# Optimization experiments

Measured on AMD Instinct MI355X. Metric: run time of the kernel, lower is better.

## Reference

```python
import jax, jax.numpy as jnp
import numpy as np

B, T, C = 2, 2048, 1024
N_HEAD, D_HEAD = 16, 64


def setup_inputs() -> dict:
    key = jax.random.key(0)
    k1, k2, k3 = jax.random.split(key, 3)
    scale_in = 1.0 / np.sqrt(C)
    return {
        "x": jax.random.normal(k1, (B, T, C), dtype=jnp.float32),
        "W_attn": jax.random.normal(k2, (C, 3 * C), dtype=jnp.float32) * scale_in,
        "b_attn": jnp.zeros((3 * C,), dtype=jnp.float32),
        "W_proj": jax.random.normal(k3, (C, C), dtype=jnp.float32) * scale_in,
        "b_proj": jnp.zeros((C,), dtype=jnp.float32),
    }


def reference(x, W_attn, b_attn, W_proj, b_proj):
    Bx, Tx, Cx = x.shape
    qkv = x @ W_attn + b_attn                       # [B,T,3C]
    q, k, v = jnp.split(qkv, 3, axis=-1)
    # [B,T,C] -> [B,H,T,Dh]
    q = q.reshape(Bx, Tx, N_HEAD, D_HEAD).transpose(0, 2, 1, 3)
    k = k.reshape(Bx, Tx, N_HEAD, D_HEAD).transpose(0, 2, 1, 3)
    v = v.reshape(Bx, Tx, N_HEAD, D_HEAD).transpose(0, 2, 1, 3)
    att = jnp.einsum("bhqd,bhkd->bhqk", q, k) * (1.0 / jnp.sqrt(D_HEAD))
    causal_mask = jnp.tril(jnp.ones((Tx, Tx), dtype=jnp.bool_))[None, None]
    att = jnp.where(causal_mask, att, -jnp.inf)
    att = jax.nn.softmax(att, axis=-1)
    y = jnp.einsum("bhqk,bhkd->bhqd", att, v)        # [B,H,T,Dh]
    y = y.transpose(0, 2, 1, 3).reshape(Bx, Tx, Cx)  # [B,T,C]
    return y @ W_proj + b_proj
```

## Files before the change

### kernel.cpp

```cpp
#include <hip/hip_runtime.h>

#define BB 2
#define TT 2048
#define CC 1024
#define NHEAD 16
#define DHEAD 64

typedef __attribute__((ext_vector_type(8))) short short8;
typedef __attribute__((ext_vector_type(8))) unsigned short ushort8;
typedef __attribute__((ext_vector_type(4))) float floatx4;
typedef __attribute__((ext_vector_type(2))) unsigned int uintx2;

__device__ inline unsigned short f32_to_bf16_rne(float f) {
  unsigned u = __builtin_bit_cast(unsigned, f);
  unsigned r = (u + 0x7FFFu + ((u >> 16) & 1u)) >> 16;
  return (unsigned short)r;
}
__device__ inline unsigned cvt_pk_bf16(float lo, float hi) {
  unsigned r;
  asm("v_cvt_pk_bf16_f32 %0, %1, %2" : "=v"(r) : "v"(lo), "v"(hi));
  return r;
}
__device__ inline void gload_lds16(const void* g, void* l) {
  __builtin_amdgcn_global_load_lds(
      (const __attribute__((address_space(1))) void*)g,
      (__attribute__((address_space(3))) void*)l, 16, 0, 0);
}

__device__ inline void transpose_tile(const float* __restrict__ W,
                                      unsigned short* __restrict__ Wt,
                                      int K, int N, int scale_cut, float scl,
                                      int bx, int by, float (*T)[33]) {
  const int tx = threadIdx.x & 31;
  const int ty = threadIdx.x >> 5;
  const int r0 = by * 32, c0 = bx * 32;
#pragma unroll
  for (int i = 0; i < 4; ++i)
    T[ty + i * 8][tx] = W[(size_t)(r0 + ty + i * 8) * N + c0 + tx];
  __syncthreads();
#pragma unroll
  for (int i = 0; i < 4; ++i) {
    const int nrow = c0 + ty + i * 8;
    const float s = (nrow < scale_cut) ? scl : 1.0f;
    Wt[(size_t)nrow * K + r0 + tx] = f32_to_bf16_rne(T[tx][ty + i * 8] * s);
  }
}

__global__ __launch_bounds__(256) void prep_kernel(
    const float* __restrict__ x, const float* __restrict__ W_attn,
    const float* __restrict__ b_attn, const float* __restrict__ W_proj,
    unsigned short* __restrict__ xb, unsigned short* __restrict__ Wat,
    unsigned short* __restrict__ Wpt, float* __restrict__ bscl, float scl) {
  __shared__ float T[32][33];
  const int id = blockIdx.x;
  if (id < 4096) {
    const int i = (id * 256 + threadIdx.x) * 4;
    float4 v = *(const float4*)(x + i);
    ushort4 o;
    o.x = f32_to_bf16_rne(v.x);
    o.y = f32_to_bf16_rne(v.y);
    o.z = f32_to_bf16_rne(v.z);
    o.w = f32_to_bf16_rne(v.w);
    *(ushort4*)(xb + i) = o;
  } else if (id < 4096 + 3072) {
    const int t = id - 4096;
    transpose_tile(W_attn, Wat, CC, 3 * CC, CC, scl, t % 96, t / 96, T);
  } else if (id < 4096 + 3072 + 1024) {
    const int t = id - (4096 + 3072);
    transpose_tile(W_proj, Wpt, CC, CC, 0, 1.0f, t % 32, t / 32, T);
  } else {
    const int i = (id - 8192) * 256 + threadIdx.x;
    if (i < 3 * CC) bscl[i] = b_attn[i] * (i < CC ? scl : 1.0f);
  }
}

__global__ __launch_bounds__(256) void transpose_v_kernel(
    const unsigned short* __restrict__ qkv, unsigned short* __restrict__ vT) {
  __shared__ unsigned short Ts[64][72];
  const int tt0 = blockIdx.x * 64;
  const int bh = blockIdx.y;
  const int h = bh & (NHEAD - 1);
  const int b = bh >> 4;
  const int tid = threadIdx.x;
  const unsigned short* src = qkv + (size_t)(b * TT) * (3 * CC) + 2 * CC + h * DHEAD;
#pragma unroll
  for (int it = 0; it < 2; ++it) {
    const int t = it * 32 + (tid >> 3);
    const int d8 = (tid & 7) * 8;
    ushort8 v = *(const ushort8*)(src + (size_t)(tt0 + t) * (3 * CC) + d8);
#pragma unroll
    for (int j = 0; j < 8; ++j) Ts[t][d8 + j] = v[j];
  }
  __syncthreads();
  unsigned short* dst = vT + ((size_t)((b * NHEAD + h) * DHEAD)) * TT;
#pragma unroll
  for (int it = 0; it < 2; ++it) {
    const int d = it * 32 + (tid >> 3);
    const int t8 = (tid & 7) * 8;
    ushort8 o;
#pragma unroll
    for (int j = 0; j < 8; ++j) o[j] = Ts[t8 + j][d];
    *(ushort8*)(dst + (size_t)d * TT + tt0 + t8) = o;
  }
}

__global__ __launch_bounds__(512, 2) void gemm256_kernel(
    const unsigned short* __restrict__ A,
    const unsigned short* __restrict__ Bt,
    const float* __restrict__ bias,
    unsigned short* __restrict__ C,
    int M, int N, int K) {
  __shared__ unsigned short SA[3][256 * 32];
  __shared__ unsigned short SB[3][256 * 32];

  const int id = blockIdx.x;
  const int xcd = id & 7;
  const int j = id >> 3;
  const int row0 = (xcd * 2 + (j >= 12 ? 1 : 0)) * 256;
  const int col0 = (j % 12) * 256;

  const int tid = threadIdx.x;
  const int w = tid >> 6;
  const int lane = tid & 63;
  const int l15 = lane & 15;
  const int l4 = lane >> 4;
  const int wr = (w >> 2) * 128;
  const int wc = (w & 3) * 64;
  const int sr = lane >> 2;
  const int sc = lane & 3;

  floatx4 acc[8][4];
#pragma unroll
  for (int m = 0; m < 8; ++m)
#pragma unroll
    for (int n = 0; n < 4; ++n) acc[m][n] = (floatx4){0.f, 0.f, 0.f, 0.f};

  auto stageA = [&](int t) {
    const int buf = t % 3;
    const int k0 = t * 32;
#pragma unroll
    for (int l = 0; l < 2; ++l) {
      const int r = w * 16 + sr + l * 128;
      gload_lds16(A + (size_t)(row0 + r) * K + k0 + ((sc ^ ((r >> 1) & 3)) * 8),
                  (char*)SA[buf] + (w * 16 + l * 128) * 64);
    }
  };
  auto stageB = [&](int t) {
    const int buf = t % 3;
    const int k0 = t * 32;
#pragma unroll
    for (int l = 0; l < 2; ++l) {
      const int r = w * 16 + sr + l * 128;
      gload_lds16(Bt + (size_t)(col0 + r) * K + k0 + ((sc ^ ((r >> 1) & 3)) * 8),
                  (char*)SB[buf] + (w * 16 + l * 128) * 64);
    }
  };

  stageA(0); stageB(0);
  stageA(1); stageB(1);
  asm volatile("s_waitcnt vmcnt(4)" ::: "memory");
  __builtin_amdgcn_s_barrier();

  const int NT = K / 32;
  for (int t = 0; t < NT; ++t) {
    const unsigned short* sa = SA[t % 3];
    const unsigned short* sb = SB[t % 3];

    short8 af[4], bf[4];
#pragma unroll
    for (int n = 0; n < 4; ++n) {
      const int rb = wc + n * 16 + l15;
      bf[n] = *(const short8*)(sb + rb * 32 + ((l4 ^ ((rb >> 1) & 3)) * 8));
    }
#pragma unroll
    for (int m = 0; m < 4; ++m) {
      const int ra = wr + m * 16 + l15;
      af[m] = *(const short8*)(sa + ra * 32 + ((l4 ^ ((ra >> 1) & 3)) * 8));
    }
    if (t + 2 < NT) stageA(t + 2);
    __builtin_amdgcn_s_barrier();
    __builtin_amdgcn_s_setprio(1);
#pragma unroll
    for (int m = 0; m < 4; ++m)
#pragma unroll
      for (int n = 0; n < 4; ++n)
        acc[m][n] = __builtin_amdgcn_mfma_f32_16x16x32_bf16(af[m], bf[n], acc[m][n], 0, 0, 0);
    __builtin_amdgcn_s_setprio(0);
    __builtin_amdgcn_s_barrier();

#pragma unroll
    for (int m = 0; m < 4; ++m) {
      const int ra = wr + 64 + m * 16 + l15;
      af[m] = *(const short8*)(sa + ra * 32 + ((l4 ^ ((ra >> 1) & 3)) * 8));
    }
    if (t + 2 < NT) stageB(t + 2);
    __builtin_amdgcn_s_barrier();
    __builtin_amdgcn_s_setprio(1);
#pragma unroll
    for (int m = 0; m < 4; ++m)
#pragma unroll
      for (int n = 0; n < 4; ++n)
        acc[4 + m][n] = __builtin_amdgcn_mfma_f32_16x16x32_bf16(af[m], bf[n], acc[4 + m][n], 0, 0, 0);
    __builtin_amdgcn_s_setprio(0);
    __builtin_amdgcn_s_barrier();

    if (t + 1 < NT) {
      if (t + 2 < NT)
        asm volatile("s_waitcnt vmcnt(4)" ::: "memory");
      else
        asm volatile("s_waitcnt vmcnt(0)" ::: "memory");
      __builtin_amdgcn_s_barrier();
    }
  }

  const int rg = l4 * 4;
#pragma unroll
  for (int m = 0; m < 8; ++m) {
#pragma unroll
    for (int n = 0; n < 4; ++n) {
      const int col = col0 + wc + n * 16 + l15;
      const float bv = bias[col];
#pragma unroll
      for (int r = 0; r < 4; ++r) {
        const int row = row0 + wr + m * 16 + rg + r;
        C[(size_t)row * N + col] = f32_to_bf16_rne(acc[m][n][r] + bv);
      }
    }
  }
}

template <bool BF16_OUT, int BN>
__global__ __launch_bounds__(256) void gemm_mfma_kernel(
    const unsigned short* __restrict__ A, const unsigned short* __restrict__ Bt,
    const float* __restrict__ bias, void* __restrict__ Cout,
    int M, int N, int K) {
  constexpr int NR = BN / 32;
  __shared__ unsigned short As[128 * 64];
  __shared__ unsigned short Bs[BN * 64];

  const int tid = threadIdx.x;
  const int wave = tid >> 6;
  const int lane = tid & 63;
  const int row0 = blockIdx.y * 128;
  const int col0 = blockIdx.x * BN;
  const int wr = (wave >> 1) * 64;
  const int wc = (wave & 1) * (BN / 2);

  floatx4 acc[4][NR];
#pragma unroll
  for (int m = 0; m < 4; ++m)
#pragma unroll
    for (int n = 0; n < NR; ++n) acc[m][n] = (floatx4){0.f, 0.f, 0.f, 0.f};

  const int sRow = lane >> 2;
  const int sK = (lane & 3) * 8;

  for (int k0 = 0; k0 < K; k0 += 64) {
#pragma unroll
    for (int kc = 0; kc < 2; ++kc) {
#pragma unroll
      for (int c = 0; c < 2; ++c) {
        const int g = c * 4 + wave;
        gload_lds16(A + (size_t)(row0 + g * 16 + sRow) * K + k0 + kc * 32 + sK,
                    (char*)As + kc * 8192 + g * 1024);
      }
      if constexpr (BN == 128) {
#pragma unroll
        for (int c = 0; c < 2; ++c) {
          const int g = c * 4 + wave;
          gload_lds16(Bt + (size_t)(col0 + g * 16 + sRow) * K + k0 + kc * 32 + sK,
                      (char*)Bs + kc * 8192 + g * 1024);
        }
      } else {
        gload_lds16(Bt + (size_t)(col0 + wave * 16 + sRow) * K + k0 + kc * 32 + sK,
                    (char*)Bs + kc * 4096 + wave * 1024);
      }
    }
    __syncthreads();

#pragma unroll
    for (int kc = 0; kc < 2; ++kc) {
      short8 af[4], bf[NR];
#pragma unroll
      for (int m = 0; m < 4; ++m)
        af[m] = *(const short8*)(As + kc * 4096 +
                                 (wr + m * 16 + (lane & 15)) * 32 + (lane >> 4) * 8);
#pragma unroll
      for (int n = 0; n < NR; ++n)
        bf[n] = *(const short8*)(Bs + kc * (BN * 32) +
                                 (wc + n * 16 + (lane & 15)) * 32 + (lane >> 4) * 8);
#pragma unroll
      for (int m = 0; m < 4; ++m)
#pragma unroll
        for (int n = 0; n < NR; ++n)
          acc[m][n] = __builtin_amdgcn_mfma_f32_16x16x32_bf16(af[m], bf[n], acc[m][n], 0, 0, 0);
    }
    __syncthreads();
  }

  const int cl = lane & 15;
  const int rg = (lane >> 4) * 4;
#pragma unroll
  for (int m = 0; m < 4; ++m) {
#pragma unroll
    for (int n = 0; n < NR; ++n) {
      const int col = col0 + wc + n * 16 + cl;
      const float bv = bias[col];
#pragma unroll
      for (int r = 0; r < 4; ++r) {
        const int row = row0 + wr + m * 16 + rg + r;
        const float v = acc[m][n][r] + bv;
        if (BF16_OUT)
          ((unsigned short*)Cout)[(size_t)row * N + col] = f32_to_bf16_rne(v);
        else
          ((float*)Cout)[(size_t)row * N + col] = v;
      }
    }
  }
}

__global__ __launch_bounds__(256) void flash_mfma_kernel(
    const unsigned short* __restrict__ qkv,
    const unsigned short* __restrict__ vT,
    unsigned short* __restrict__ y) {
  __shared__ unsigned short Ks[2][64 * 64];
  __shared__ unsigned short Vs[2][64 * 64];
  __shared__ unsigned short Ps[4][16 * 64];

  const int id = blockIdx.x;
  const int xcd = id & 7;
  const int grp = (id >> 3) & 3;
  const int p = id >> 5;
  const int bh = xcd * 4 + grp;
  const int qtA = 31 - p, qtB = p;
  const int ntA = qtA + 1, ntB = qtB + 1;

  const int h = bh & (NHEAD - 1);
  const int b = bh >> 4;
  const int tid = threadIdx.x;
  const int wq = tid >> 6;
  const int lane = tid & 63;
  const int l15 = lane & 15;
  const int l4 = lane >> 4;
  const int srow = lane >> 3;
  const int schunk = lane & 7;

  const size_t baseQ = (size_t)(b * TT) * (3 * CC) + h * DHEAD;
  const size_t baseK = baseQ + CC;
  const size_t vbase = (size_t)((b * NHEAD + h) * DHEAD) * TT;

  short8 aqA[2], aqB[2];
  {
    const unsigned short* qp =
        qkv + baseQ + (size_t)(qtA * 64 + wq * 16 + l15) * (3 * CC) + l4 * 8;
    aqA[0] = *(const short8*)(qp);
    aqA[1] = *(const short8*)(qp + 32);
    const unsigned short* qp2 =
        qkv + baseQ + (size_t)(qtB * 64 + wq * 16 + l15) * (3 * CC) + l4 * 8;
    aqB[0] = *(const short8*)(qp2);
    aqB[1] = *(const short8*)(qp2 + 32);
  }

  floatx4 accT[4];
  float m_i = -1e30f, l_i = 0.f;
#pragma unroll
  for (int n = 0; n < 4; ++n) accT[n] = (floatx4){0.f, 0.f, 0.f, 0.f};

  auto stage = [&](int KT, int BUF) {
#pragma unroll
    for (int it = 0; it < 2; ++it) {
      const int blk = it * 4 + wq;
      const int grow = blk * 8 + srow;
      gload_lds16(qkv + baseK + (size_t)(KT * 64 + grow) * (3 * CC) +
                      (schunk ^ srow) * 8,
                  (char*)Ks[BUF] + blk * 1024);
      gload_lds16(vT + vbase + (size_t)grow * TT + KT * 64 + (schunk ^ srow) * 8,
                  (char*)Vs[BUF] + blk * 1024);
    }
  };

  auto epilogue = [&](int qt) {
    char* Pw = (char*)Ps[wq];
    const float inv = 1.0f / l_i;
#pragma unroll
    for (int nd = 0; nd < 4; ++nd) {
      uintx2 dw;
      dw[0] = cvt_pk_bf16(accT[nd][0] * inv, accT[nd][1] * inv);
      dw[1] = cvt_pk_bf16(accT[nd][2] * inv, accT[nd][3] * inv);
      const int c = nd * 2 + (l4 >> 1);
      *(uintx2*)(Pw + l15 * 128 + ((c ^ (l15 & 7)) * 16) + (l4 & 1) * 8) = dw;
    }
    asm volatile("s_waitcnt lgkmcnt(0)" ::: "memory");
#pragma unroll
    for (int ch = 0; ch < 2; ++ch) {
      const int q16 = lane >> 2;
      const int c = ch * 4 + (lane & 3);
      ushort8 o = *(const ushort8*)(Pw + q16 * 128 + ((c ^ (q16 & 7)) * 16));
      const int qg = qt * 64 + wq * 16 + q16;
      *(ushort8*)(y + (size_t)(b * TT + qg) * CC + h * DHEAD + c * 8) = o;
    }
  };

  const int nt_total = ntA + ntB;

  stage(0, 0);
  asm volatile("s_waitcnt vmcnt(0)" ::: "memory");
  __builtin_amdgcn_s_barrier();

  for (int t = 0; t < nt_total; ++t) {
    const bool phB = (t >= ntA);
    const int kt = phB ? t - ntA : t;
    const int qminw = (phB ? qtB : qtA) * 64 + wq * 16;
    const int cur = t & 1;
    if (t + 1 < nt_total)
      stage((t + 1 >= ntA) ? t + 1 - ntA : t + 1, cur ^ 1);

    floatx4 sa[4];
#pragma unroll
    for (int f = 0; f < 4; ++f) sa[f] = (floatx4){0.f, 0.f, 0.f, 0.f};

    __builtin_amdgcn_s_setprio(1);
#pragma unroll
    for (int kc = 0; kc < 2; ++kc) {
      const short8 aq = phB ? aqB[kc] : aqA[kc];
#pragma unroll
      for (int f = 0; f < 4; ++f) {
        const int row = 16 * f + l15;
        short8 bk = *(const short8*)(Ks[cur] + row * 64 +
                                     ((kc * 4 + l4) ^ (row & 7)) * 8);
        sa[f] = __builtin_amdgcn_mfma_f32_16x16x32_bf16(bk, aq, sa[f], 0, 0, 0);
      }
    }
    __builtin_amdgcn_s_setprio(0);

    const int qg = qminw + l15;
    if (kt * 64 + 63 > qminw) {
#pragma unroll
      for (int f = 0; f < 4; ++f)
#pragma unroll
        for (int r = 0; r < 4; ++r) {
          const int kg = kt * 64 + f * 16 + l4 * 4 + r;
          if (kg > qg) sa[f][r] = -1e30f;
        }
    }
    float rm = -1e30f;
#pragma unroll
    for (int f = 0; f < 4; ++f)
      rm = fmaxf(rm, fmaxf(fmaxf(sa[f][0], sa[f][1]), fmaxf(sa[f][2], sa[f][3])));
    rm = fmaxf(rm, __shfl_xor(rm, 16, 64));
    rm = fmaxf(rm, __shfl_xor(rm, 32, 64));

    float rs = 0.f;
    if (__all(rm <= m_i + 8.0f)) {
#pragma unroll
      for (int f = 0; f < 4; ++f)
#pragma unroll
        for (int r = 0; r < 4; ++r) {
          const float pv = __builtin_amdgcn_exp2f(sa[f][r] - m_i);
          sa[f][r] = pv;
          rs += pv;
        }
      rs += __shfl_xor(rs, 16, 64);
      rs += __shfl_xor(rs, 32, 64);
      l_i += rs;
    } else {
      const float mn = fmaxf(m_i, rm);
      const float scale = __builtin_amdgcn_exp2f(m_i - mn);
#pragma unroll
      for (int f = 0; f < 4; ++f)
#pragma unroll
        for (int r = 0; r < 4; ++r) {
          const float pv = __builtin_amdgcn_exp2f(sa[f][r] - mn);
          sa[f][r] = pv;
          rs += pv;
        }
      rs += __shfl_xor(rs, 16, 64);
      rs += __shfl_xor(rs, 32, 64);
      l_i = l_i * scale + rs;
      m_i = mn;
#pragma unroll
      for (int nd = 0; nd < 4; ++nd) accT[nd] *= scale;
    }

    char* Pg = (char*)Ps[wq];
#pragma unroll
    for (int f = 0; f < 4; ++f) {
      uintx2 dw;
      dw[0] = cvt_pk_bf16(sa[f][0], sa[f][1]);
      dw[1] = cvt_pk_bf16(sa[f][2], sa[f][3]);
      const int c = f * 2 + (l4 >> 1);
      *(uintx2*)(Pg + l15 * 128 + ((c ^ (l15 & 7)) * 16) + (l4 & 1) * 8) = dw;
    }
    asm volatile("s_waitcnt lgkmcnt(0)" ::: "memory");

    short8 pb[2];
#pragma unroll
    for (int kc = 0; kc < 2; ++kc) {
      const int c = kc * 4 + l4;
      pb[kc] = *(const short8*)(Pg + l15 * 128 + ((c ^ (l15 & 7)) * 16));
    }

    __builtin_amdgcn_s_setprio(1);
#pragma unroll
    for (int kc = 0; kc < 2; ++kc) {
#pragma unroll
      for (int nd = 0; nd < 4; ++nd) {
        const int row = 16 * nd + l15;
        short8 vb = *(const short8*)(Vs[cur] + row * 64 +
                                     ((kc * 4 + l4) ^ (row & 7)) * 8);
        accT[nd] = __builtin_amdgcn_mfma_f32_16x16x32_bf16(vb, pb[kc], accT[nd], 0, 0, 0);
      }
    }
    __builtin_amdgcn_s_setprio(0);

    asm volatile("s_waitcnt vmcnt(0)" ::: "memory");
    __builtin_amdgcn_s_barrier();

    if (t == ntA - 1) {
      epilogue(qtA);
      m_i = -1e30f;
      l_i = 0.f;
#pragma unroll
      for (int n = 0; n < 4; ++n) accT[n] = (floatx4){0.f, 0.f, 0.f, 0.f};
    }
  }

  epilogue(qtB);
}

extern "C" void kernel_launch(void* const* d_in, const int* in_sizes, int n_in,
                              void* d_out, int out_size, void* d_ws, size_t ws_size,
                              hipStream_t stream) {
  const float* x      = (const float*)d_in[0];
  const float* W_attn = (const float*)d_in[1];
  const float* b_attn = (const float*)d_in[2];
  const float* W_proj = (const float*)d_in[3];
  const float* b_proj = (const float*)d_in[4];
  float* out = (float*)d_out;

  const int M = BB * TT;
  const float SCL = 0.125f * 1.44269504089f;

  unsigned short* qkvb = (unsigned short*)d_ws;
  unsigned short* xb   = qkvb + (size_t)M * 3 * CC;
  unsigned short* Wat  = xb + (size_t)M * CC;
  unsigned short* Wpt  = Wat + (size_t)3 * CC * CC;
  unsigned short* yb   = Wpt + (size_t)CC * CC;
  unsigned short* vTb  = yb + (size_t)M * CC;
  float* bscl = (float*)(vTb + (size_t)BB * NHEAD * DHEAD * TT);

  prep_kernel<<<8204, 256, 0, stream>>>(x, W_attn, b_attn, W_proj,
                                        xb, Wat, Wpt, bscl, SCL);

  gemm256_kernel<<<192, 512, 0, stream>>>(xb, Wat, bscl, qkvb, M, 3 * CC, CC);

  {
    dim3 grid(TT / 64, BB * NHEAD);
    transpose_v_kernel<<<grid, 256, 0, stream>>>(qkvb, vTb);
  }

  flash_mfma_kernel<<<512, 256, 0, stream>>>(qkvb, vTb, yb);

  {
    dim3 grid(CC / 64, M / 128);
    gemm_mfma_kernel<false, 64><<<grid, 256, 0, stream>>>(
        yb, Wpt, b_proj, out, M, CC, CC);
  }
}
```

Measured before the change: 120.4 us.

## Pipeline output projection GEMM with triple-buffered LDS, swizzle and XCD-aware tiling

Replaces the output projection GEMM with a new kernel that stages K in 32-wide slices through a three-deep LDS ring. Loads for slice t+2 are issued before the MFMAs of slice t, and waits use vmcnt counting, so each step needs one barrier instead of two. LDS rows are XOR-swizzled to avoid bank conflicts, and block indices are remapped so each XCD works on a fixed pair of column tiles, which improves L2 reuse of the weights. The costs are more complex wait/barrier logic and a hardcoded grid of 512 blocks.

```diff
diff --git a/kernel.cpp b/kernel.cpp
--- a/kernel.cpp
+++ b/kernel.cpp
@@ -229,91 +229,104 @@
   }
 }
 
-template <bool BF16_OUT, int BN>
-__global__ __launch_bounds__(256) void gemm_mfma_kernel(
-    const unsigned short* __restrict__ A, const unsigned short* __restrict__ Bt,
-    const float* __restrict__ bias, void* __restrict__ Cout,
+__global__ __launch_bounds__(256) void gemm2_kernel(
+    const unsigned short* __restrict__ A,
+    const unsigned short* __restrict__ Bt,
+    const float* __restrict__ bias,
+    float* __restrict__ C,
     int M, int N, int K) {
-  constexpr int NR = BN / 32;
-  __shared__ unsigned short As[128 * 64];
-  __shared__ unsigned short Bs[BN * 64];
+  __shared__ unsigned short SA[3][128 * 32];
+  __shared__ unsigned short SB[3][64 * 32];
+
+  const int id = blockIdx.x;
+  const int xcd = id & 7;
+  const int j = id >> 3;
+  const int col0 = (xcd * 2 + (j >= 32 ? 1 : 0)) * 64;
+  const int row0 = (j & 31) * 128;
 
   const int tid = threadIdx.x;
-  const int wave = tid >> 6;
+  const int w = tid >> 6;
   const int lane = tid & 63;
-  const int row0 = blockIdx.y * 128;
-  const int col0 = blockIdx.x * BN;
-  const int wr = (wave >> 1) * 64;
-  const int wc = (wave & 1) * (BN / 2);
-
-  floatx4 acc[4][NR];
+  const int l15 = lane & 15;
+  const int l4 = lane >> 4;
+  const int wr = (w >> 1) * 64;
+  const int wc = (w & 1) * 32;
+  const int sr = lane >> 2;
+  const int sc = lane & 3;
+
+  floatx4 acc[4][2];
 #pragma unroll
   for (int m = 0; m < 4; ++m)
 #pragma unroll
-    for (int n = 0; n < NR; ++n) acc[m][n] = (floatx4){0.f, 0.f, 0.f, 0.f};
-
-  const int sRow = lane >> 2;
-  const int sK = (lane & 3) * 8;
-
-  for (int k0 = 0; k0 < K; k0 += 64) {
-#pragma unroll
-    for (int kc = 0; kc < 2; ++kc) {
-#pragma unroll
-      for (int c = 0; c < 2; ++c) {
-        const int g = c * 4 + wave;
-        gload_lds16(A + (size_t)(row0 + g * 16 + sRow) * K + k0 + kc * 32 + sK,
-                    (char*)As + kc * 8192 + g * 1024);
-      }
-      if constexpr (BN == 128) {
-#pragma unroll
-        for (int c = 0; c < 2; ++c) {
-          const int g = c * 4 + wave;
-          gload_lds16(Bt + (size_t)(col0 + g * 16 + sRow) * K + k0 + kc * 32 + sK,
-                      (char*)Bs + kc * 8192 + g * 1024);
-        }
-      } else {
-        gload_lds16(Bt + (size_t)(col0 + wave * 16 + sRow) * K + k0 + kc * 32 + sK,
-                    (char*)Bs + kc * 4096 + wave * 1024);
-      }
-    }
-    __syncthreads();
-
-#pragma unroll
-    for (int kc = 0; kc < 2; ++kc) {
-      short8 af[4], bf[NR];
-#pragma unroll
-      for (int m = 0; m < 4; ++m)
-        af[m] = *(const short8*)(As + kc * 4096 +
-                                 (wr + m * 16 + (lane & 15)) * 32 + (lane >> 4) * 8);
-#pragma unroll
-      for (int n = 0; n < NR; ++n)
-        bf[n] = *(const short8*)(Bs + kc * (BN * 32) +
-                                 (wc + n * 16 + (lane & 15)) * 32 + (lane >> 4) * 8);
-#pragma unroll
-      for (int m = 0; m < 4; ++m)
-#pragma unroll
-        for (int n = 0; n < NR; ++n)
-          acc[m][n] = __builtin_amdgcn_mfma_f32_16x16x32_bf16(af[m], bf[n], acc[m][n], 0, 0, 0);
-    }
-    __syncthreads();
-  }
-
-  const int cl = lane & 15;
-  const int rg = (lane >> 4) * 4;
+    for (int n = 0; n < 2; ++n) acc[m][n] = (floatx4){0.f, 0.f, 0.f, 0.f};
+
+  auto stage = [&](int t) {
+    const int buf = t % 3;
+    const int k0 = t * 32;
+#pragma unroll
+    for (int l = 0; l < 2; ++l) {
+      const int r = w * 16 + sr + l * 64;
+      gload_lds16(A + (size_t)(row0 + r) * K + k0 + ((sc ^ ((r >> 1) & 3)) * 8),
+                  (char*)SA[buf] + (w * 16 + l * 64) * 64);
+    }
+    {
+      const int r = w * 16 + sr;
+      gload_lds16(Bt + (size_t)(col0 + r) * K + k0 + ((sc ^ ((r >> 1) & 3)) * 8),
+                  (char*)SB[buf] + (w * 16) * 64);
+    }
+  };
+
+  stage(0);
+  stage(1);
+  asm volatile("s_waitcnt vmcnt(3)" ::: "memory");
+  __builtin_amdgcn_s_barrier();
+
+  const int NT = K / 32;
+  for (int t = 0; t < NT; ++t) {
+    const unsigned short* sa = SA[t % 3];
+    const unsigned short* sb = SB[t % 3];
+
+    short8 af[4], bf[2];
+#pragma unroll
+    for (int n = 0; n < 2; ++n) {
+      const int rb = wc + n * 16 + l15;
+      bf[n] = *(const short8*)(sb + rb * 32 + ((l4 ^ ((rb >> 1) & 3)) * 8));
+    }
+#pragma unroll
+    for (int m = 0; m < 4; ++m) {
+      const int ra = wr + m * 16 + l15;
+      af[m] = *(const short8*)(sa + ra * 32 + ((l4 ^ ((ra >> 1) & 3)) * 8));
+    }
+    if (t + 2 < NT) stage(t + 2);
+
+    __builtin_amdgcn_s_setprio(1);
+#pragma unroll
+    for (int m = 0; m < 4; ++m)
+#pragma unroll
+      for (int n = 0; n < 2; ++n)
+        acc[m][n] = __builtin_amdgcn_mfma_f32_16x16x32_bf16(af[m], bf[n], acc[m][n], 0, 0, 0);
+    __builtin_amdgcn_s_setprio(0);
+
+    if (t + 1 < NT) {
+      if (t + 2 < NT)
+        asm volatile("s_waitcnt vmcnt(3)" ::: "memory");
+      else
+        asm volatile("s_waitcnt vmcnt(0)" ::: "memory");
+      __builtin_amdgcn_s_barrier();
+    }
+  }
+
+  const int rg = l4 * 4;
 #pragma unroll
   for (int m = 0; m < 4; ++m) {
 #pragma unroll
-    for (int n = 0; n < NR; ++n) {
-      const int col = col0 + wc + n * 16 + cl;
+    for (int n = 0; n < 2; ++n) {
+      const int col = col0 + wc + n * 16 + l15;
       const float bv = bias[col];
 #pragma unroll
       for (int r = 0; r < 4; ++r) {
         const int row = row0 + wr + m * 16 + rg + r;
-        const float v = acc[m][n][r] + bv;
-        if (BF16_OUT)
-          ((unsigned short*)Cout)[(size_t)row * N + col] = f32_to_bf16_rne(v);
-        else
-          ((float*)Cout)[(size_t)row * N + col] = v;
+        C[(size_t)row * N + col] = acc[m][n][r] + bv;
       }
     }
   }
@@ -561,9 +574,5 @@
 
   flash_mfma_kernel<<<512, 256, 0, stream>>>(qkvb, vTb, yb);
 
-  {
-    dim3 grid(CC / 64, M / 128);
-    gemm_mfma_kernel<false, 64><<<grid, 256, 0, stream>>>(
-        yb, Wpt, b_proj, out, M, CC, CC);
-  }
-}
+  gemm2_kernel<<<512, 256, 0, stream>>>(yb, Wpt, b_proj, out, M, CC, CC);
+}
```

Result: no change. 119.1 us (-1.1%).
